# Optimization experiments

Measured on AMD Instinct MI355X. Metric: run time of the kernel, lower is better.

## Reference

```python
import jax, jax.numpy as jnp
import numpy as np

T, K, E, H, I = 1024, 8, 64, 1024, 512
CAP_FACTOR = 4  # capacity = CAP_FACTOR * T*K/E; overflow prob ~0 for uniform routing


def setup_inputs() -> dict:
    key = jax.random.key(0)
    k1, k2, k3, k4, k5 = jax.random.split(key, 5)
    hidden_states = jax.random.normal(k1, (T, H), dtype=jnp.float32)
    top_k_indices = jax.random.randint(k2, (T, K), 0, E, dtype=jnp.int32)
    top_k_weights = jax.random.uniform(k3, (T, K), dtype=jnp.float32)
    gate_up_proj = jax.random.normal(k4, (E, 2 * I, H), dtype=jnp.float32) * 0.02
    down_proj = jax.random.normal(k5, (E, H, I), dtype=jnp.float32) * 0.02
    return {
        "hidden_states": hidden_states,
        "top_k_indices": top_k_indices,
        "top_k_weights": top_k_weights,
        "gate_up_proj": gate_up_proj,
        "down_proj": down_proj,
    }


def reference(hidden_states, top_k_indices, top_k_weights, gate_up_proj, down_proj):
    # Grouped-GEMM MoE dispatch/combine. Same math as the torch module:
    # per (token, slot) pair, route token to expert idx[t,k], apply
    # SiLU-gated MLP of that expert, scale by weights[t,k], sum over k.
    Tn, Hn = hidden_states.shape
    Kn = top_k_indices.shape[1]
    En = gate_up_proj.shape[0]
    In = down_proj.shape[2]
    C = CAP_FACTOR * (Tn * Kn) // En  # per-expert capacity (static)

    flat_idx = top_k_indices.reshape(Tn * Kn)               # pair -> expert
    m = jax.nn.one_hot(flat_idx, En, dtype=jnp.int32)       # [TK, E]
    pos = jnp.cumsum(m, axis=0) - 1                          # position within expert
    pos = jnp.take_along_axis(pos, flat_idx[:, None], axis=1)[:, 0]
    pos = jnp.minimum(pos, C - 1)                            # safety clamp (never hit for C >> load)
    slot = flat_idx * C + pos                                # [TK]

    # Dispatch: scatter each (token, k) copy into its expert bucket
    x_rep = jnp.repeat(hidden_states, Kn, axis=0)            # [TK, H], row t*K+k = token t
    xd = jnp.zeros((En * C, Hn), hidden_states.dtype).at[slot].set(x_rep)
    xd = xd.reshape(En, C, Hn)

    # Per-expert SiLU-gated MLP as grouped GEMMs
    gu = jnp.einsum('ech,eoh->eco', xd, gate_up_proj)        # [E, C, 2I]
    gate, up = gu[..., :In], gu[..., In:]
    h = jax.nn.silu(gate) * up                               # [E, C, I]
    yd = jnp.einsum('eci,ehi->ech', h, down_proj)            # [E, C, H]

    # Combine: gather back per pair, weight, and sum over the K slots
    y_pairs = yd.reshape(En * C, Hn)[slot]                   # [TK, H]
    w = top_k_weights.reshape(Tn * Kn, 1)
    return (y_pairs * w).reshape(Tn, Kn, Hn).sum(axis=1)     # [T, H]
```

## Files before the change

### kernel.cpp

```cpp
#include <hip/hip_runtime.h>

#define Tn 1024
#define Kn 8
#define En 64
#define Hn 1024
#define In 512
#define RCAP 256

typedef __attribute__((ext_vector_type(8))) short bf16x8;
typedef __attribute__((ext_vector_type(4))) float f32x4;

__device__ __forceinline__ short f2bf(float f) {
  unsigned u = __float_as_uint(f);
  unsigned r = (u + 0x7FFFu + ((u >> 16) & 1u)) >> 16;
  return (short)r;
}
__device__ __forceinline__ float bf2f(short s) {
  return __uint_as_float(((unsigned)(unsigned short)s) << 16);
}
__device__ __forceinline__ void load_lds16(const void* g, void* l) {
  __builtin_amdgcn_global_load_lds(
      (const __attribute__((address_space(1))) void*)g,
      (__attribute__((address_space(3))) void*)l, 16, 0, 0);
}

__global__ __launch_bounds__(256) void k_route(
    const float* __restrict__ hs, const int* __restrict__ idx,
    int* __restrict__ cnt, int* __restrict__ p2r, short* __restrict__ Xe) {
  const int pair = blockIdx.x * 4 + (threadIdx.x >> 6);
  const int lane = threadIdx.x & 63;
  const int e = idx[pair];
  int p = 0;
  if (lane == 0) p = atomicAdd(&cnt[e], 1);
  p = __shfl(p, 0);
  if (lane == 0) p2r[pair] = e * RCAP + min(p, RCAP - 1);
  if (p < RCAP) {
    const int t = pair >> 3;
    const float* src = hs + (size_t)t * Hn;
    short* dst = Xe + (size_t)(e * RCAP + p) * Hn;
#pragma unroll
    for (int j = 0; j < 4; ++j) {
      const int c0 = j * 256 + lane * 4;
      float4 v = *(const float4*)&src[c0];
      short4 s;
      s.x = f2bf(v.x); s.y = f2bf(v.y); s.z = f2bf(v.z); s.w = f2bf(v.w);
      *(short4*)&dst[c0] = s;
    }
  }
}

__global__ __launch_bounds__(256) void k_gemm1(
    const short* __restrict__ Xe, const float* __restrict__ gup,
    const int* __restrict__ cnt, short* __restrict__ hb) {
  const int e = blockIdx.z, mb = blockIdx.y, nb = blockIdx.x;
  const int ne = min(cnt[e], RCAP);
  if (mb * 128 >= ne) return;
  __shared__ short As[128][32];
  __shared__ short Bs[128][32];
  const int tid = threadIdx.x;
  const int lane = tid & 63, wid = tid >> 6;
  const int base_row = e * RCAP + mb * 128;

  const short* aptr[2];
  short* ldst[2];
#pragma unroll
  for (int it = 0; it < 2; ++it) {
    const int seg = wid * 2 + it;
    const int r = seg * 16 + (lane >> 2);
    const int cb = (lane & 3) * 8;
    aptr[it] = &Xe[(size_t)(base_row + r) * Hn + cb];
    ldst[it] = &As[seg * 16][0];
  }
  const float* bsrc[4];
  short* bdst[4];
#pragma unroll
  for (int it = 0; it < 4; ++it) {
    const int c2 = it * 256 + tid;
    const int row = c2 >> 3, cg = c2 & 7;
    const int o = (row < 64) ? (nb * 64 + row) : (In + nb * 64 + (row - 64));
    bsrc[it] = &gup[(size_t)e * (2 * In) * Hn + (size_t)o * Hn + cg * 4];
    bdst[it] = &Bs[row][cg * 4];
  }

  f32x4 acc[2][8];
#pragma unroll
  for (int mf = 0; mf < 2; ++mf)
#pragma unroll
    for (int nf = 0; nf < 8; ++nf) acc[mf][nf] = (f32x4)(0.f);

  for (int k0 = 0; k0 < Hn; k0 += 32) {
#pragma unroll
    for (int it = 0; it < 2; ++it) load_lds16(aptr[it] + k0, ldst[it]);
#pragma unroll
    for (int it = 0; it < 4; ++it) {
      float4 v = *(const float4*)(bsrc[it] + k0);
      short4 s;
      s.x = f2bf(v.x); s.y = f2bf(v.y); s.z = f2bf(v.z); s.w = f2bf(v.w);
      *(short4*)bdst[it] = s;
    }
    __syncthreads();
    bf16x8 a[2], b[8];
#pragma unroll
    for (int mf = 0; mf < 2; ++mf)
      a[mf] = *(const bf16x8*)&As[wid * 32 + mf * 16 + (lane & 15)][(lane >> 4) * 8];
#pragma unroll
    for (int nf = 0; nf < 8; ++nf)
      b[nf] = *(const bf16x8*)&Bs[nf * 16 + (lane & 15)][(lane >> 4) * 8];
#pragma unroll
    for (int nf = 0; nf < 8; ++nf)
#pragma unroll
      for (int mf = 0; mf < 2; ++mf)
        acc[mf][nf] = __builtin_amdgcn_mfma_f32_16x16x32_bf16(a[mf], b[nf], acc[mf][nf], 0, 0, 0);
    __syncthreads();
  }

#pragma unroll
  for (int mf = 0; mf < 2; ++mf)
#pragma unroll
    for (int nf = 0; nf < 4; ++nf)
#pragma unroll
      for (int r = 0; r < 4; ++r) {
        const float g = acc[mf][nf][r];
        const float u = acc[mf][nf + 4][r];
        const float hv = (g / (1.f + __expf(-g))) * u;
        const int rl = wid * 32 + mf * 16 + (lane >> 4) * 4 + r;
        const int hc = nb * 64 + nf * 16 + (lane & 15);
        hb[(size_t)(base_row + rl) * In + hc] = f2bf(hv);
      }
}

__global__ __launch_bounds__(256) void k_gemm2(
    const short* __restrict__ hb, const float* __restrict__ dp,
    const int* __restrict__ cnt, short* __restrict__ yd) {
  const int e = blockIdx.z, mb = blockIdx.y, nb = blockIdx.x;
  const int ne = min(cnt[e], RCAP);
  if (mb * 128 >= ne) return;
  __shared__ short As[128][32];
  __shared__ short Bs[128][32];
  const int tid = threadIdx.x;
  const int lane = tid & 63, wid = tid >> 6;
  const int base_row = e * RCAP + mb * 128;

  const short* aptr[2];
  short* ldst[2];
#pragma unroll
  for (int it = 0; it < 2; ++it) {
    const int seg = wid * 2 + it;
    const int r = seg * 16 + (lane >> 2);
    const int cb = (lane & 3) * 8;
    aptr[it] = &hb[(size_t)(base_row + r) * In + cb];
    ldst[it] = &As[seg * 16][0];
  }
  const float* bsrc[4];
  short* bdst[4];
#pragma unroll
  for (int it = 0; it < 4; ++it) {
    const int c2 = it * 256 + tid;
    const int row = c2 >> 3, cg = c2 & 7;
    const int o = nb * 128 + row;
    bsrc[it] = &dp[((size_t)e * Hn + o) * In + cg * 4];
    bdst[it] = &Bs[row][cg * 4];
  }

  f32x4 acc[2][8];
#pragma unroll
  for (int mf = 0; mf < 2; ++mf)
#pragma unroll
    for (int nf = 0; nf < 8; ++nf) acc[mf][nf] = (f32x4)(0.f);

  for (int k0 = 0; k0 < In; k0 += 32) {
#pragma unroll
    for (int it = 0; it < 2; ++it) load_lds16(aptr[it] + k0, ldst[it]);
#pragma unroll
    for (int it = 0; it < 4; ++it) {
      float4 v = *(const float4*)(bsrc[it] + k0);
      short4 s;
      s.x = f2bf(v.x); s.y = f2bf(v.y); s.z = f2bf(v.z); s.w = f2bf(v.w);
      *(short4*)bdst[it] = s;
    }
    __syncthreads();
    bf16x8 a[2], b[8];
#pragma unroll
    for (int mf = 0; mf < 2; ++mf)
      a[mf] = *(const bf16x8*)&As[wid * 32 + mf * 16 + (lane & 15)][(lane >> 4) * 8];
#pragma unroll
    for (int nf = 0; nf < 8; ++nf)
      b[nf] = *(const bf16x8*)&Bs[nf * 16 + (lane & 15)][(lane >> 4) * 8];
#pragma unroll
    for (int nf = 0; nf < 8; ++nf)
#pragma unroll
      for (int mf = 0; mf < 2; ++mf)
        acc[mf][nf] = __builtin_amdgcn_mfma_f32_16x16x32_bf16(a[mf], b[nf], acc[mf][nf], 0, 0, 0);
    __syncthreads();
  }

#pragma unroll
  for (int mf = 0; mf < 2; ++mf)
#pragma unroll
    for (int nf = 0; nf < 8; ++nf)
#pragma unroll
      for (int r = 0; r < 4; ++r) {
        const int rl = wid * 32 + mf * 16 + (lane >> 4) * 4 + r;
        const int col = nb * 128 + nf * 16 + (lane & 15);
        yd[(size_t)(base_row + rl) * Hn + col] = f2bf(acc[mf][nf][r]);
      }
}

__global__ __launch_bounds__(256) void k_combine(
    const short* __restrict__ yd, const int* __restrict__ p2r,
    const float* __restrict__ tkw, float* __restrict__ out) {
  const int t = blockIdx.x;
  const int c = threadIdx.x * 4;
  float4 acc = make_float4(0.f, 0.f, 0.f, 0.f);
#pragma unroll
  for (int k = 0; k < Kn; ++k) {
    const int i = t * Kn + k;
    const int row = p2r[i];
    const float w = tkw[i];
    short4 v = *(const short4*)&yd[(size_t)row * Hn + c];
    acc.x += w * bf2f(v.x);
    acc.y += w * bf2f(v.y);
    acc.z += w * bf2f(v.z);
    acc.w += w * bf2f(v.w);
  }
  *(float4*)&out[(size_t)t * Hn + c] = acc;
}

extern "C" void kernel_launch(void* const* d_in, const int* in_sizes, int n_in,
                              void* d_out, int out_size, void* d_ws, size_t ws_size,
                              hipStream_t stream) {
  const float* hs = (const float*)d_in[0];
  const int* idx = (const int*)d_in[1];
  const float* tkw = (const float*)d_in[2];
  const float* gup = (const float*)d_in[3];
  const float* dp = (const float*)d_in[4];
  float* out = (float*)d_out;

  char* w = (char*)d_ws;
  int* cnt = (int*)(w + 0);
  int* p2r = (int*)(w + 4096);
  short* Xe = (short*)(w + (1u << 20));
  short* hb = (short*)(w + 34603008u);
  short* yd = (short*)(w + 51380224u);

  hipMemsetAsync(cnt, 0, En * sizeof(int), stream);
  k_route<<<dim3((Tn * Kn) / 4), dim3(256), 0, stream>>>(hs, idx, cnt, p2r, Xe);
  k_gemm1<<<dim3(In / 64, RCAP / 128, En), dim3(256), 0, stream>>>(Xe, gup, cnt, hb);
  k_gemm2<<<dim3(Hn / 128, RCAP / 128, En), dim3(256), 0, stream>>>(hb, dp, cnt, yd);
  k_combine<<<dim3(Tn), dim3(256), 0, stream>>>(yd, p2r, tkw, out);
}
```

Baseline: 573.3 us.

## Double-buffer LDS tiles in both expert GEMMs to overlap loads with MFMA

Both grouped GEMM kernels now use two LDS buffers for the A and B tiles. The next K-tile's global loads (A via direct-to-LDS, B as fp32 into registers) are issued before the current tile's MFMAs, and B is converted to bf16 and stored to the other buffer afterwards, leaving one barrier per iteration instead of two. The aim is to hide global memory latency behind matrix math, at the cost of doubled LDS (32 KB per block) and more live registers, which may lower occupancy.

```diff
diff --git a/kernel.cpp b/kernel.cpp
--- a/kernel.cpp
+++ b/kernel.cpp
@@ -55,31 +55,31 @@
   const int e = blockIdx.z, mb = blockIdx.y, nb = blockIdx.x;
   const int ne = min(cnt[e], RCAP);
   if (mb * 128 >= ne) return;
-  __shared__ short As[128][32];
-  __shared__ short Bs[128][32];
+  __shared__ short As[2][128][32];
+  __shared__ short Bs[2][128][32];
   const int tid = threadIdx.x;
   const int lane = tid & 63, wid = tid >> 6;
   const int base_row = e * RCAP + mb * 128;
 
   const short* aptr[2];
-  short* ldst[2];
+  int aoff[2];
 #pragma unroll
   for (int it = 0; it < 2; ++it) {
     const int seg = wid * 2 + it;
     const int r = seg * 16 + (lane >> 2);
     const int cb = (lane & 3) * 8;
     aptr[it] = &Xe[(size_t)(base_row + r) * Hn + cb];
-    ldst[it] = &As[seg * 16][0];
+    aoff[it] = seg * 16;
   }
   const float* bsrc[4];
-  short* bdst[4];
+  int brow[4], bcol[4];
 #pragma unroll
   for (int it = 0; it < 4; ++it) {
     const int c2 = it * 256 + tid;
     const int row = c2 >> 3, cg = c2 & 7;
     const int o = (row < 64) ? (nb * 64 + row) : (In + nb * 64 + (row - 64));
     bsrc[it] = &gup[(size_t)e * (2 * In) * Hn + (size_t)o * Hn + cg * 4];
-    bdst[it] = &Bs[row][cg * 4];
+    brow[it] = row; bcol[it] = cg * 4;
   }
 
   f32x4 acc[2][8];
@@ -88,29 +88,49 @@
 #pragma unroll
     for (int nf = 0; nf < 8; ++nf) acc[mf][nf] = (f32x4)(0.f);
 
-  for (int k0 = 0; k0 < Hn; k0 += 32) {
-#pragma unroll
-    for (int it = 0; it < 2; ++it) load_lds16(aptr[it] + k0, ldst[it]);
-#pragma unroll
-    for (int it = 0; it < 4; ++it) {
-      float4 v = *(const float4*)(bsrc[it] + k0);
-      short4 s;
-      s.x = f2bf(v.x); s.y = f2bf(v.y); s.z = f2bf(v.z); s.w = f2bf(v.w);
-      *(short4*)bdst[it] = s;
-    }
-    __syncthreads();
+  const int NT = Hn / 32;
+  float4 bv[4];
+#pragma unroll
+  for (int it = 0; it < 2; ++it) load_lds16(aptr[it], &As[0][aoff[it]][0]);
+#pragma unroll
+  for (int it = 0; it < 4; ++it) bv[it] = *(const float4*)(bsrc[it]);
+#pragma unroll
+  for (int it = 0; it < 4; ++it) {
+    short4 s;
+    s.x = f2bf(bv[it].x); s.y = f2bf(bv[it].y); s.z = f2bf(bv[it].z); s.w = f2bf(bv[it].w);
+    *(short4*)&Bs[0][brow[it]][bcol[it]] = s;
+  }
+  __syncthreads();
+
+  for (int t = 0; t < NT; ++t) {
+    const int cur = t & 1, nxt = cur ^ 1;
+    const int k1 = (t + 1) * 32;
+    if (t + 1 < NT) {
+#pragma unroll
+      for (int it = 0; it < 2; ++it) load_lds16(aptr[it] + k1, &As[nxt][aoff[it]][0]);
+#pragma unroll
+      for (int it = 0; it < 4; ++it) bv[it] = *(const float4*)(bsrc[it] + k1);
+    }
     bf16x8 a[2], b[8];
 #pragma unroll
     for (int mf = 0; mf < 2; ++mf)
-      a[mf] = *(const bf16x8*)&As[wid * 32 + mf * 16 + (lane & 15)][(lane >> 4) * 8];
-#pragma unroll
-    for (int nf = 0; nf < 8; ++nf)
-      b[nf] = *(const bf16x8*)&Bs[nf * 16 + (lane & 15)][(lane >> 4) * 8];
+      a[mf] = *(const bf16x8*)&As[cur][wid * 32 + mf * 16 + (lane & 15)][(lane >> 4) * 8];
+#pragma unroll
+    for (int nf = 0; nf < 8; ++nf)
+      b[nf] = *(const bf16x8*)&Bs[cur][nf * 16 + (lane & 15)][(lane >> 4) * 8];
 #pragma unroll
     for (int nf = 0; nf < 8; ++nf)
 #pragma unroll
       for (int mf = 0; mf < 2; ++mf)
         acc[mf][nf] = __builtin_amdgcn_mfma_f32_16x16x32_bf16(a[mf], b[nf], acc[mf][nf], 0, 0, 0);
+    if (t + 1 < NT) {
+#pragma unroll
+      for (int it = 0; it < 4; ++it) {
+        short4 s;
+        s.x = f2bf(bv[it].x); s.y = f2bf(bv[it].y); s.z = f2bf(bv[it].z); s.w = f2bf(bv[it].w);
+        *(short4*)&Bs[nxt][brow[it]][bcol[it]] = s;
+      }
+    }
     __syncthreads();
   }
 
@@ -135,31 +155,31 @@
   const int e = blockIdx.z, mb = blockIdx.y, nb = blockIdx.x;
   const int ne = min(cnt[e], RCAP);
   if (mb * 128 >= ne) return;
-  __shared__ short As[128][32];
-  __shared__ short Bs[128][32];
+  __shared__ short As[2][128][32];
+  __shared__ short Bs[2][128][32];
   const int tid = threadIdx.x;
   const int lane = tid & 63, wid = tid >> 6;
   const int base_row = e * RCAP + mb * 128;
 
   const short* aptr[2];
-  short* ldst[2];
+  int aoff[2];
 #pragma unroll
   for (int it = 0; it < 2; ++it) {
     const int seg = wid * 2 + it;
     const int r = seg * 16 + (lane >> 2);
     const int cb = (lane & 3) * 8;
     aptr[it] = &hb[(size_t)(base_row + r) * In + cb];
-    ldst[it] = &As[seg * 16][0];
+    aoff[it] = seg * 16;
   }
   const float* bsrc[4];
-  short* bdst[4];
+  int brow[4], bcol[4];
 #pragma unroll
   for (int it = 0; it < 4; ++it) {
     const int c2 = it * 256 + tid;
     const int row = c2 >> 3, cg = c2 & 7;
     const int o = nb * 128 + row;
     bsrc[it] = &dp[((size_t)e * Hn + o) * In + cg * 4];
-    bdst[it] = &Bs[row][cg * 4];
+    brow[it] = row; bcol[it] = cg * 4;
   }
 
   f32x4 acc[2][8];
@@ -168,29 +188,49 @@
 #pragma unroll
     for (int nf = 0; nf < 8; ++nf) acc[mf][nf] = (f32x4)(0.f);
 
-  for (int k0 = 0; k0 < In; k0 += 32) {
-#pragma unroll
-    for (int it = 0; it < 2; ++it) load_lds16(aptr[it] + k0, ldst[it]);
-#pragma unroll
-    for (int it = 0; it < 4; ++it) {
-      float4 v = *(const float4*)(bsrc[it] + k0);
-      short4 s;
-      s.x = f2bf(v.x); s.y = f2bf(v.y); s.z = f2bf(v.z); s.w = f2bf(v.w);
-      *(short4*)bdst[it] = s;
-    }
-    __syncthreads();
+  const int NT = In / 32;
+  float4 bv[4];
+#pragma unroll
+  for (int it = 0; it < 2; ++it) load_lds16(aptr[it], &As[0][aoff[it]][0]);
+#pragma unroll
+  for (int it = 0; it < 4; ++it) bv[it] = *(const float4*)(bsrc[it]);
+#pragma unroll
+  for (int it = 0; it < 4; ++it) {
+    short4 s;
+    s.x = f2bf(bv[it].x); s.y = f2bf(bv[it].y); s.z = f2bf(bv[it].z); s.w = f2bf(bv[it].w);
+    *(short4*)&Bs[0][brow[it]][bcol[it]] = s;
+  }
+  __syncthreads();
+
+  for (int t = 0; t < NT; ++t) {
+    const int cur = t & 1, nxt = cur ^ 1;
+    const int k1 = (t + 1) * 32;
+    if (t + 1 < NT) {
+#pragma unroll
+      for (int it = 0; it < 2; ++it) load_lds16(aptr[it] + k1, &As[nxt][aoff[it]][0]);
+#pragma unroll
+      for (int it = 0; it < 4; ++it) bv[it] = *(const float4*)(bsrc[it] + k1);
+    }
     bf16x8 a[2], b[8];
 #pragma unroll
     for (int mf = 0; mf < 2; ++mf)
-      a[mf] = *(const bf16x8*)&As[wid * 32 + mf * 16 + (lane & 15)][(lane >> 4) * 8];
-#pragma unroll
-    for (int nf = 0; nf < 8; ++nf)
-      b[nf] = *(const bf16x8*)&Bs[nf * 16 + (lane & 15)][(lane >> 4) * 8];
+      a[mf] = *(const bf16x8*)&As[cur][wid * 32 + mf * 16 + (lane & 15)][(lane >> 4) * 8];
+#pragma unroll
+    for (int nf = 0; nf < 8; ++nf)
+      b[nf] = *(const bf16x8*)&Bs[cur][nf * 16 + (lane & 15)][(lane >> 4) * 8];
 #pragma unroll
     for (int nf = 0; nf < 8; ++nf)
 #pragma unroll
       for (int mf = 0; mf < 2; ++mf)
         acc[mf][nf] = __builtin_amdgcn_mfma_f32_16x16x32_bf16(a[mf], b[nf], acc[mf][nf], 0, 0, 0);
+    if (t + 1 < NT) {
+#pragma unroll
+      for (int it = 0; it < 4; ++it) {
+        short4 s;
+        s.x = f2bf(bv[it].x); s.y = f2bf(bv[it].y); s.z = f2bf(bv[it].z); s.w = f2bf(bv[it].w);
+        *(short4*)&Bs[nxt][brow[it]][bcol[it]] = s;
+      }
+    }
     __syncthreads();
   }
 
```

Result: slower. 586.6 us (+2.3%).

## Pre-convert expert weights to bf16 and double-buffer direct-to-LDS GEMM loads

Applied to the files above, without the earlier changes.

Adds a conversion kernel that turns the fp32 gate_up and down weights into bf16 in the workspace on every call. New GEMM kernels then load both operands with global_load_lds into double-buffered shared memory, so the next K-tile is fetched while the current one runs on MFMA, and the per-iteration register conversion stalls go away. This only happens when the workspace is large enough; otherwise the old fp32 kernels still run. The cost is an extra full pass over the weights (read fp32, write bf16, read bf16 again), which adds DRAM traffic in return for better latency hiding.

```diff
diff --git a/kernel.cpp b/kernel.cpp
--- a/kernel.cpp
+++ b/kernel.cpp
@@ -22,6 +22,27 @@
   __builtin_amdgcn_global_load_lds(
       (const __attribute__((address_space(1))) void*)g,
       (__attribute__((address_space(3))) void*)l, 16, 0, 0);
+}
+
+__device__ __forceinline__ void cvt8(const float* __restrict__ src,
+                                     short* __restrict__ dst) {
+  float4 v0 = *(const float4*)src;
+  float4 v1 = *(const float4*)(src + 4);
+  bf16x8 s;
+  s[0] = f2bf(v0.x); s[1] = f2bf(v0.y); s[2] = f2bf(v0.z); s[3] = f2bf(v0.w);
+  s[4] = f2bf(v1.x); s[5] = f2bf(v1.y); s[6] = f2bf(v1.z); s[7] = f2bf(v1.w);
+  *(bf16x8*)dst = s;
+}
+
+__global__ __launch_bounds__(256) void k_convert(
+    const float* __restrict__ gup, const float* __restrict__ dp,
+    short* __restrict__ wgu, short* __restrict__ wdp) {
+  const size_t NG = (size_t)En * 2 * In * Hn;
+  const size_t ND = (size_t)En * Hn * In;
+  const size_t stride = (size_t)gridDim.x * 256 * 8;
+  size_t base = ((size_t)blockIdx.x * 256 + threadIdx.x) * 8;
+  for (size_t i = base; i < NG; i += stride) cvt8(&gup[i], &wgu[i]);
+  for (size_t i = base; i < ND; i += stride) cvt8(&dp[i], &wdp[i]);
 }
 
 __global__ __launch_bounds__(256) void k_route(
@@ -49,7 +70,165 @@
   }
 }
 
-__global__ __launch_bounds__(256) void k_gemm1(
+__global__ __launch_bounds__(256) void k_gemm1_bf(
+    const short* __restrict__ Xe, const short* __restrict__ wgu,
+    const int* __restrict__ cnt, short* __restrict__ hb) {
+  const int e = blockIdx.z, mb = blockIdx.y, nb = blockIdx.x;
+  const int ne = min(cnt[e], RCAP);
+  if (mb * 128 >= ne) return;
+  __shared__ short As[2][128][32];
+  __shared__ short Bs[2][128][32];
+  const int tid = threadIdx.x;
+  const int lane = tid & 63, wid = tid >> 6;
+  const int base_row = e * RCAP + mb * 128;
+
+  const short* aptr[2];
+  const short* bptr[2];
+  int soff[2];
+#pragma unroll
+  for (int it = 0; it < 2; ++it) {
+    const int seg = wid * 2 + it;
+    const int r = seg * 16 + (lane >> 2);
+    const int ce = (lane & 3) * 8;
+    aptr[it] = &Xe[(size_t)(base_row + r) * Hn + ce];
+    const int o = (seg < 4) ? (nb * 64 + seg * 16 + (lane >> 2))
+                            : (In + nb * 64 + (seg - 4) * 16 + (lane >> 2));
+    bptr[it] = &wgu[(size_t)e * (2 * In) * Hn + (size_t)o * Hn + ce];
+    soff[it] = seg * 16;
+  }
+
+  f32x4 acc[2][8];
+#pragma unroll
+  for (int mf = 0; mf < 2; ++mf)
+#pragma unroll
+    for (int nf = 0; nf < 8; ++nf) acc[mf][nf] = (f32x4)(0.f);
+
+  const int NT = Hn / 32;
+#pragma unroll
+  for (int it = 0; it < 2; ++it) {
+    load_lds16(aptr[it], &As[0][soff[it]][0]);
+    load_lds16(bptr[it], &Bs[0][soff[it]][0]);
+  }
+  __syncthreads();
+
+  for (int t = 0; t < NT; ++t) {
+    const int cur = t & 1, nxt = cur ^ 1;
+    if (t + 1 < NT) {
+      const int k1 = (t + 1) * 32;
+#pragma unroll
+      for (int it = 0; it < 2; ++it) {
+        load_lds16(aptr[it] + k1, &As[nxt][soff[it]][0]);
+        load_lds16(bptr[it] + k1, &Bs[nxt][soff[it]][0]);
+      }
+    }
+    bf16x8 a[2], b[8];
+#pragma unroll
+    for (int mf = 0; mf < 2; ++mf)
+      a[mf] = *(const bf16x8*)&As[cur][wid * 32 + mf * 16 + (lane & 15)][(lane >> 4) * 8];
+#pragma unroll
+    for (int nf = 0; nf < 8; ++nf)
+      b[nf] = *(const bf16x8*)&Bs[cur][nf * 16 + (lane & 15)][(lane >> 4) * 8];
+#pragma unroll
+    for (int nf = 0; nf < 8; ++nf)
+#pragma unroll
+      for (int mf = 0; mf < 2; ++mf)
+        acc[mf][nf] = __builtin_amdgcn_mfma_f32_16x16x32_bf16(a[mf], b[nf], acc[mf][nf], 0, 0, 0);
+    __syncthreads();
+  }
+
+#pragma unroll
+  for (int mf = 0; mf < 2; ++mf)
+#pragma unroll
+    for (int nf = 0; nf < 4; ++nf)
+#pragma unroll
+      for (int r = 0; r < 4; ++r) {
+        const float g = acc[mf][nf][r];
+        const float u = acc[mf][nf + 4][r];
+        const float hv = (g / (1.f + __expf(-g))) * u;
+        const int rl = wid * 32 + mf * 16 + (lane >> 4) * 4 + r;
+        const int hc = nb * 64 + nf * 16 + (lane & 15);
+        hb[(size_t)(base_row + rl) * In + hc] = f2bf(hv);
+      }
+}
+
+__global__ __launch_bounds__(256) void k_gemm2_bf(
+    const short* __restrict__ hb, const short* __restrict__ wdp,
+    const int* __restrict__ cnt, short* __restrict__ yd) {
+  const int e = blockIdx.z, mb = blockIdx.y, nb = blockIdx.x;
+  const int ne = min(cnt[e], RCAP);
+  if (mb * 128 >= ne) return;
+  __shared__ short As[2][128][32];
+  __shared__ short Bs[2][128][32];
+  const int tid = threadIdx.x;
+  const int lane = tid & 63, wid = tid >> 6;
+  const int base_row = e * RCAP + mb * 128;
+
+  const short* aptr[2];
+  const short* bptr[2];
+  int soff[2];
+#pragma unroll
+  for (int it = 0; it < 2; ++it) {
+    const int seg = wid * 2 + it;
+    const int r = seg * 16 + (lane >> 2);
+    const int ce = (lane & 3) * 8;
+    aptr[it] = &hb[(size_t)(base_row + r) * In + ce];
+    const int o = nb * 128 + seg * 16 + (lane >> 2);
+    bptr[it] = &wdp[((size_t)e * Hn + o) * In + ce];
+    soff[it] = seg * 16;
+  }
+
+  f32x4 acc[2][8];
+#pragma unroll
+  for (int mf = 0; mf < 2; ++mf)
+#pragma unroll
+    for (int nf = 0; nf < 8; ++nf) acc[mf][nf] = (f32x4)(0.f);
+
+  const int NT = In / 32;
+#pragma unroll
+  for (int it = 0; it < 2; ++it) {
+    load_lds16(aptr[it], &As[0][soff[it]][0]);
+    load_lds16(bptr[it], &Bs[0][soff[it]][0]);
+  }
+  __syncthreads();
+
+  for (int t = 0; t < NT; ++t) {
+    const int cur = t & 1, nxt = cur ^ 1;
+    if (t + 1 < NT) {
+      const int k1 = (t + 1) * 32;
+#pragma unroll
+      for (int it = 0; it < 2; ++it) {
+        load_lds16(aptr[it] + k1, &As[nxt][soff[it]][0]);
+        load_lds16(bptr[it] + k1, &Bs[nxt][soff[it]][0]);
+      }
+    }
+    bf16x8 a[2], b[8];
+#pragma unroll
+    for (int mf = 0; mf < 2; ++mf)
+      a[mf] = *(const bf16x8*)&As[cur][wid * 32 + mf * 16 + (lane & 15)][(lane >> 4) * 8];
+#pragma unroll
+    for (int nf = 0; nf < 8; ++nf)
+      b[nf] = *(const bf16x8*)&Bs[cur][nf * 16 + (lane & 15)][(lane >> 4) * 8];
+#pragma unroll
+    for (int nf = 0; nf < 8; ++nf)
+#pragma unroll
+      for (int mf = 0; mf < 2; ++mf)
+        acc[mf][nf] = __builtin_amdgcn_mfma_f32_16x16x32_bf16(a[mf], b[nf], acc[mf][nf], 0, 0, 0);
+    __syncthreads();
+  }
+
+#pragma unroll
+  for (int mf = 0; mf < 2; ++mf)
+#pragma unroll
+    for (int nf = 0; nf < 8; ++nf)
+#pragma unroll
+      for (int r = 0; r < 4; ++r) {
+        const int rl = wid * 32 + mf * 16 + (lane >> 4) * 4 + r;
+        const int col = nb * 128 + nf * 16 + (lane & 15);
+        yd[(size_t)(base_row + rl) * Hn + col] = f2bf(acc[mf][nf][r]);
+      }
+}
+
+__global__ __launch_bounds__(256) void k_gemm1_f32(
     const short* __restrict__ Xe, const float* __restrict__ gup,
     const int* __restrict__ cnt, short* __restrict__ hb) {
   const int e = blockIdx.z, mb = blockIdx.y, nb = blockIdx.x;
@@ -129,7 +308,7 @@
       }
 }
 
-__global__ __launch_bounds__(256) void k_gemm2(
+__global__ __launch_bounds__(256) void k_gemm2_f32(
     const short* __restrict__ hb, const float* __restrict__ dp,
     const int* __restrict__ cnt, short* __restrict__ yd) {
   const int e = blockIdx.z, mb = blockIdx.y, nb = blockIdx.x;
@@ -239,13 +418,27 @@
   char* w = (char*)d_ws;
   int* cnt = (int*)(w + 0);
   int* p2r = (int*)(w + 4096);
-  short* Xe = (short*)(w + (1u << 20));
-  short* hb = (short*)(w + 34603008u);
-  short* yd = (short*)(w + 51380224u);
+  short* Xe = (short*)(w + 1048576u);
+
+  const bool big = ws_size >= 252706816ull;
 
   hipMemsetAsync(cnt, 0, En * sizeof(int), stream);
   k_route<<<dim3((Tn * Kn) / 4), dim3(256), 0, stream>>>(hs, idx, cnt, p2r, Xe);
-  k_gemm1<<<dim3(In / 64, RCAP / 128, En), dim3(256), 0, stream>>>(Xe, gup, cnt, hb);
-  k_gemm2<<<dim3(Hn / 128, RCAP / 128, En), dim3(256), 0, stream>>>(hb, dp, cnt, yd);
-  k_combine<<<dim3(Tn), dim3(256), 0, stream>>>(yd, p2r, tkw, out);
-}
+
+  if (big) {
+    short* hb  = (short*)(w + 34603008u);
+    short* wgu = (short*)(w + 51380224u);
+    short* wdp = (short*)(w + 185597952u);
+    short* yd  = (short*)(w + 51380224u);
+    k_convert<<<dim3(2048), dim3(256), 0, stream>>>(gup, dp, wgu, wdp);
+    k_gemm1_bf<<<dim3(In / 64, RCAP / 128, En), dim3(256), 0, stream>>>(Xe, wgu, cnt, hb);
+    k_gemm2_bf<<<dim3(Hn / 128, RCAP / 128, En), dim3(256), 0, stream>>>(hb, wdp, cnt, yd);
+    k_combine<<<dim3(Tn), dim3(256), 0, stream>>>(yd, p2r, tkw, out);
+  } else {
+    short* hb = (short*)(w + 34603008u);
+    short* yd = (short*)(w + 51380224u);
+    k_gemm1_f32<<<dim3(In / 64, RCAP / 128, En), dim3(256), 0, stream>>>(Xe, gup, cnt, hb);
+    k_gemm2_f32<<<dim3(Hn / 128, RCAP / 128, En), dim3(256), 0, stream>>>(hb, dp, cnt, yd);
+    k_combine<<<dim3(Tn), dim3(256), 0, stream>>>(yd, p2r, tkw, out);
+  }
+}
```

Measured after the change: 638.1 us. 1.11x slower.
